# Kernel tuning notes

Measured on AMD Instinct MI355X. Metric: run time of the kernel, lower is better.

## Reference

```python
import jax, jax.numpy as jnp
import numpy as np

H = 12          # num attention heads
D = 768         # hidden size
DH = D // H     # head dim = 64

def setup_inputs() -> dict:
    key = jax.random.key(0)
    ks = jax.random.split(key, 9)
    B, N = 8, 1024
    s = 0.02
    return {
        "hidden_states": jax.random.normal(ks[0], (B, N, D), jnp.float32),
        "Wq": jax.random.normal(ks[1], (D, D), jnp.float32) * s,
        "bq": jnp.zeros((D,), jnp.float32),
        "Wk": jax.random.normal(ks[2], (D, D), jnp.float32) * s,
        "bk": jnp.zeros((D,), jnp.float32),
        "Wv": jax.random.normal(ks[3], (D, D), jnp.float32) * s,
        "bv": jnp.zeros((D,), jnp.float32),
        "Wo": jax.random.normal(ks[4], (D, D), jnp.float32) * s,
        "bo": jnp.zeros((D,), jnp.float32),
    }

def _split_heads(x):
    # [B, N, D] -> [B, H, N, DH]
    B, N, _ = x.shape
    return x.reshape(B, N, H, DH).transpose(0, 2, 1, 3)

def reference(hidden_states, Wq, bq, Wk, bk, Wv, bv, Wo, bo):
    # torch Linear: y = x @ W.T + b
    q = _split_heads(hidden_states @ Wq.T + bq)
    k = _split_heads(hidden_states @ Wk.T + bk)
    v = _split_heads(hidden_states @ Wv.T + bv)
    scale = 1.0 / jnp.sqrt(jnp.asarray(DH, hidden_states.dtype))
    scores = jnp.einsum("bhqd,bhkd->bhqk", q, k) * scale
    probs = jax.nn.softmax(scores, axis=-1)
    ctx = jnp.einsum("bhqk,bhkd->bhqd", probs, v)
    B, _, N, _ = ctx.shape
    ctx = ctx.transpose(0, 2, 1, 3).reshape(B, N, D)
    return ctx @ Wo.T + bo
```

## Files before the change

kernel.cpp:

```cpp
#include <hip/hip_runtime.h>

typedef unsigned short u16;
typedef unsigned int   u32;
typedef unsigned long long u64;
typedef __attribute__((ext_vector_type(8))) short bf16x8;
typedef __attribute__((ext_vector_type(4))) float f32x4;
typedef __attribute__((address_space(3))) u32 lds_u32;
typedef __attribute__((address_space(1))) u32 gbl_u32;

#define MFMA16(a,b,c) __builtin_amdgcn_mfma_f32_16x16x32_bf16((a),(b),(c),0,0,0)
#define QSCALE 0.1803368801111204f

#define WAIT3 do{ asm volatile("s_waitcnt vmcnt(3)" ::: "memory"); }while(0)
#define WAIT4 do{ asm volatile("s_waitcnt vmcnt(4)" ::: "memory"); }while(0)
#define WAIT0 do{ asm volatile("s_waitcnt vmcnt(0)" ::: "memory"); }while(0)
#define SCHED __builtin_amdgcn_sched_barrier(0)
#define BARR  __builtin_amdgcn_s_barrier()

__device__ __forceinline__ u16 f2bf(float f){
  u32 u = __builtin_bit_cast(u32, f);
  u32 r = u + 0x7fffu + ((u>>16)&1u);
  return (u16)(r>>16);
}
__device__ __forceinline__ float bf2f(u16 h){
  return __builtin_bit_cast(float, (u32)h<<16);
}

union V8 { u16 s[8]; uint4 v; };

__global__ __launch_bounds__(256) void cvt_all(const float* __restrict__ hs,
    const float* __restrict__ Wq, const float* __restrict__ Wk,
    const float* __restrict__ Wv, const float* __restrict__ Wo,
    u16* __restrict__ hsb, u16* __restrict__ wqkv, u16* __restrict__ woh)
{
  const int bid = blockIdx.x;
  if (bid < 3072){
    int i = bid*256 + threadIdx.x;
    const float4* p = (const float4*)(hs + (size_t)i*8);
    float4 a = p[0], b = p[1];
    V8 t;
    t.s[0]=f2bf(a.x); t.s[1]=f2bf(a.y); t.s[2]=f2bf(a.z); t.s[3]=f2bf(a.w);
    t.s[4]=f2bf(b.x); t.s[5]=f2bf(b.y); t.s[6]=f2bf(b.z); t.s[7]=f2bf(b.w);
    *(uint4*)(hsb + (size_t)i*8) = t.v;
    return;
  }
  const int r = bid - 3072;
  const int seg = r / 288;
  const int off = (r - seg*288)*256 + threadIdx.x;
  const float* src = seg==0?Wq: seg==1?Wk: seg==2?Wv: Wo;
  const float4* p = (const float4*)(src + (size_t)off*8);
  float4 a = p[0], b = p[1];
  float xs[8] = {a.x,a.y,a.z,a.w,b.x,b.y,b.z,b.w};
  V8 t;
  #pragma unroll
  for (int j=0;j<8;++j) t.s[j]=f2bf(xs[j]);
  if (seg < 3) *(uint4*)(wqkv + (size_t)seg*589824 + (size_t)off*8) = t.v;
  else         *(uint4*)(woh  + (size_t)off*8) = t.v;
}

__global__ __launch_bounds__(512) void mm_qkv(const u16* __restrict__ A, const u16* __restrict__ Bp,
    const float* __restrict__ bq, const float* __restrict__ bk, const float* __restrict__ bvv,
    u16* __restrict__ Oq, u16* __restrict__ Ok, u16* __restrict__ Ov)
{
  __shared__ u16 P[3][12288];
  const int bid = blockIdx.x;
  const int sid = (bid & 7)*72 + (bid >> 3);
  const int mb = sid/9, nb = sid - mb*9;
  const int m0 = mb*128, n0 = nb*256;
  const int tid = threadIdx.x;
  const int lane = tid&63, wid = tid>>6;
  const int wr = wid>>2, wc = wid&3;
  const int fr = lane&15, fg = lane>>4;

  const char* Ab = (const char*)A;
  const char* Bb = (const char*)Bp;
  const char* sp[3];
  #pragma unroll
  for (int c=0;c<3;++c){
    int ci = c*512 + tid;
    if (ci < 512){
      int line = ci>>3, slot = ci&7;
      int d = slot ^ (line&7);
      int row = 2*line + (d>>2);
      sp[c] = Ab + (size_t)(m0+row)*1536 + (d&3)*16;
    } else {
      int i = ci - 512;
      int line = i>>3, slot = i&7;
      int d = slot ^ (line&7);
      int row = 2*line + (d>>2);
      sp[c] = Bb + (size_t)(n0+row)*1536 + (d&3)*16;
    }
  }
  const int sl = (((fr&1)<<2) + fg) ^ (fr>>1);
  const int aoff = (fr&~1)*64 + sl*16 + wr*4096;
  const int boff = 8192 + (fr&~1)*64 + sl*16 + wc*4096;

  f32x4 zz = {0.f,0.f,0.f,0.f};
  f32x4 acc[4][4];
  #pragma unroll
  for (int i=0;i<4;++i)
    #pragma unroll
    for (int j=0;j<4;++j) acc[i][j]=zz;

  auto STAGE = [&](int t, int b){
    char* dst0 = (char*)P[b];
    #pragma unroll
    for (int c=0;c<3;++c)
      __builtin_amdgcn_global_load_lds((const gbl_u32*)(sp[c] + (size_t)t*64),
        (lds_u32*)(dst0 + c*8192 + wid*1024), 16, 0, 0);
  };
  auto COMPUTE = [&](int b){
    const char* pb = (const char*)P[b];
    bf16x8 bfr[4];
    #pragma unroll
    for (int nt=0;nt<4;++nt)
      bfr[nt] = *(const bf16x8*)(pb + boff + nt*1024);
    #pragma unroll
    for (int mt=0;mt<4;++mt){
      bf16x8 af = *(const bf16x8*)(pb + aoff + mt*1024);
      #pragma unroll
      for (int nt=0;nt<4;++nt)
        acc[mt][nt] = MFMA16(af, bfr[nt], acc[mt][nt]);
    }
  };

  STAGE(0, 0); STAGE(1, 1);
  int cb = 0;
  for (int t=0; t<24; ++t){
    if (t < 23) WAIT3; else WAIT0;
    BARR; SCHED;
    if (t < 22){
      int sb = cb + 2; if (sb >= 3) sb -= 3;
      STAGE(t+2, sb);
    }
    __builtin_amdgcn_s_setprio(1);
    COMPUTE(cb);
    __builtin_amdgcn_s_setprio(0);
    cb = (cb == 2) ? 0 : cb + 1;
  }

  const int seg = nb/3;
  const float* bias = seg==0?bq: seg==1?bk:bvv;
  const float sc = (seg==0) ? QSCALE : 1.0f;
  if (seg < 2){
    u16* O = seg==0?Oq:Ok;
    #pragma unroll
    for (int mt=0;mt<4;++mt){
      #pragma unroll
      for (int nt=0;nt<4;++nt){
        int colw = n0 + wc*64 + nt*16 + fr - seg*768;
        float bz = bias[colw];
        int hh = colw>>6, d = colw&63;
        #pragma unroll
        for (int rr=0;rr<4;++rr){
          int row = m0 + wr*64 + mt*16 + fg*4 + rr;
          int b = row>>10, nn = row&1023;
          O[((size_t)(b*12+hh)<<16) + (size_t)nn*64 + d] = f2bf((acc[mt][nt][rr] + bz) * sc);
        }
      }
    }
  } else {
    #pragma unroll
    for (int mt=0;mt<4;++mt){
      #pragma unroll
      for (int nt=0;nt<4;++nt){
        int colw = n0 + wc*64 + nt*16 + fr - 1536;
        float bz = bias[colw];
        int hh = colw>>6, d = colw&63;
        int row0 = m0 + wr*64 + mt*16 + fg*4;
        int b = row0>>10, nn = row0&1023;
        union { u16 h[4]; u64 q; } pk;
        #pragma unroll
        for (int rr=0;rr<4;++rr) pk.h[rr] = f2bf(acc[mt][nt][rr] + bz);
        *(u64*)&Ov[((size_t)(b*12+hh)<<16) + (size_t)d*1024 + nn] = pk.q;
      }
    }
  }
}

__global__ __launch_bounds__(256) void mm_o(const u16* __restrict__ A, const u16* __restrict__ Bp,
                                            const float* __restrict__ bias, float* __restrict__ O)
{
  __shared__ u16 P[3][8192];
  const int bid = blockIdx.x;
  const int sid = (bid & 7)*48 + (bid >> 3);
  const int mb = sid/6, nb = sid - mb*6;
  const int m0 = mb*128, n0 = nb*128;
  const int tid = threadIdx.x;
  const int lane = tid&63, wid = tid>>6;
  const int wr = wid>>1, wc = wid&1;
  const int fr = lane&15, fg = lane>>4;

  const char* Ab = (const char*)A;
  const char* Bb = (const char*)Bp;
  const char* sp[4];
  #pragma unroll
  for (int c=0;c<4;++c){
    int ci = c*256 + tid;
    int row = ci>>3, slot = ci&7;
    int d = slot ^ (row&7);
    if (d < 4) sp[c] = Ab + (size_t)(m0+row)*1536 + d*16;
    else       sp[c] = Bb + (size_t)(n0+row)*1536 + (d-4)*16;
  }
  const int sA = (fg ^ (fr&7)) << 4;
  const int sB = sA ^ 64;

  f32x4 zz = {0.f,0.f,0.f,0.f};
  f32x4 acc[4][4];
  #pragma unroll
  for (int i=0;i<4;++i)
    #pragma unroll
    for (int j=0;j<4;++j) acc[i][j]=zz;

  auto STAGE = [&](int t, int b){
    char* dst0 = (char*)P[b];
    #pragma unroll
    for (int c=0;c<4;++c)
      __builtin_amdgcn_global_load_lds((const gbl_u32*)(sp[c] + (size_t)t*64),
        (lds_u32*)(dst0 + c*4096 + wid*1024), 16, 0, 0);
  };
  auto COMPUTE = [&](int b){
    const char* pb = (const char*)P[b];
    bf16x8 bfr[4];
    #pragma unroll
    for (int nt=0;nt<4;++nt)
      bfr[nt] = *(const bf16x8*)(pb + (wc*64+nt*16+fr)*128 + sB);
    #pragma unroll
    for (int mt=0;mt<4;++mt){
      bf16x8 af = *(const bf16x8*)(pb + (wr*64+mt*16+fr)*128 + sA);
      #pragma unroll
      for (int nt=0;nt<4;++nt)
        acc[mt][nt] = MFMA16(af, bfr[nt], acc[mt][nt]);
    }
  };

  STAGE(0, 0); STAGE(1, 1);
  int cb = 0;
  for (int t=0; t<24; ++t){
    if (t < 23) WAIT4; else WAIT0;
    BARR; SCHED;
    if (t < 22){
      int sb = cb + 2; if (sb >= 3) sb -= 3;
      STAGE(t+2, sb);
    }
    __builtin_amdgcn_s_setprio(1);
    COMPUTE(cb);
    __builtin_amdgcn_s_setprio(0);
    cb = (cb == 2) ? 0 : cb + 1;
  }

  #pragma unroll
  for (int mt=0;mt<4;++mt){
    #pragma unroll
    for (int nt=0;nt<4;++nt){
      int colb = n0 + wc*64 + nt*16 + fr;
      float bz = bias[colb];
      #pragma unroll
      for (int rr=0;rr<4;++rr){
        int row = m0 + wr*64 + mt*16 + fg*4 + rr;
        O[(size_t)row*768 + colb] = acc[mt][nt][rr] + bz;
      }
    }
  }
}

__global__ __launch_bounds__(256) void attn(const u16* __restrict__ qh, const u16* __restrict__ kh,
                                            const u16* __restrict__ vh, u16* __restrict__ ch)
{
  __shared__ u16 Kb[2][4096];
  __shared__ u16 Vb[2][4096];
  __shared__ u16 Ps[4][32][72];
  const int tid=threadIdx.x, w=tid>>6, lane=tid&63;
  const int fr=lane&15, fg=lane>>4;
  const int bh=blockIdx.x, qt=blockIdx.y;
  const size_t base=(size_t)bh<<16;
  const int q0=qt*128 + w*32;

  const char* kbase = (const char*)(kh + base);
  const char* vbase = (const char*)(vh + base);

  int koff[2], voff[2];
  #pragma unroll
  for (int c=0;c<2;++c){
    int ci = c*256 + tid;
    int row = ci>>3;
    int colp = ((ci&7)*16) ^ ((row&7)<<4);
    koff[c] = row*128  + colp;
    voff[c] = row*2048 + colp;
  }

  bf16x8 qf[2][2];
  #pragma unroll
  for (int mt=0;mt<2;++mt)
    #pragma unroll
    for (int ks=0;ks<2;++ks)
      qf[mt][ks] = *(const bf16x8*)&qh[base + (size_t)(q0+mt*16+fr)*64 + ks*32 + fg*8];

  const int swz = (fr&7)<<4;
  int lowD[2];
  #pragma unroll
  for (int ks=0;ks<2;++ks) lowD[ks] = (ks*64 + fg*16) ^ swz;
  const int frbase = fr*128;

  f32x4 zz = {0.f,0.f,0.f,0.f};
  f32x4 o[2][4];
  float lr[2] = {0.f, 0.f};
  #pragma unroll
  for (int mt=0;mt<2;++mt)
    #pragma unroll
    for (int j=0;j<4;++j) o[mt][j]=zz;

  {
    #pragma unroll
    for (int c=0;c<2;++c){
      __builtin_amdgcn_global_load_lds((const gbl_u32*)(kbase + koff[c]),
        (lds_u32*)((char*)&Kb[0][0] + c*4096 + w*1024), 16, 0, 0);
      __builtin_amdgcn_global_load_lds((const gbl_u32*)(vbase + voff[c]),
        (lds_u32*)((char*)&Vb[0][0] + c*4096 + w*1024), 16, 0, 0);
    }
  }
  __syncthreads();

  for (int kt=0; kt<16; ++kt){
    const int buf = kt & 1;
    {
      const int ktn = (kt+1) & 15;
      const char* kt_ = kbase + ktn*8192;
      const char* vt_ = vbase + ktn*128;
      #pragma unroll
      for (int c=0;c<2;++c){
        __builtin_amdgcn_global_load_lds((const gbl_u32*)(kt_ + koff[c]),
          (lds_u32*)((char*)&Kb[buf^1][0] + c*4096 + w*1024), 16, 0, 0);
        __builtin_amdgcn_global_load_lds((const gbl_u32*)(vt_ + voff[c]),
          (lds_u32*)((char*)&Vb[buf^1][0] + c*4096 + w*1024), 16, 0, 0);
      }
    }

    f32x4 s[2][4];
    #pragma unroll
    for (int mt=0;mt<2;++mt)
      #pragma unroll
      for (int j=0;j<4;++j) s[mt][j]=zz;
    const char* kb = (const char*)&Kb[buf][0];
    __builtin_amdgcn_s_setprio(1);
    #pragma unroll
    for (int ct=0;ct<4;++ct){
      #pragma unroll
      for (int ks=0;ks<2;++ks){
        bf16x8 kf = *(const bf16x8*)(kb + ct*2048 + frbase + lowD[ks]);
        s[0][ct]=MFMA16(kf,qf[0][ks],s[0][ct]);
        s[1][ct]=MFMA16(kf,qf[1][ks],s[1][ct]);
      }
    }
    __builtin_amdgcn_s_setprio(0);

    #pragma unroll
    for (int mt=0;mt<2;++mt){
      float lsum = 0.f;
      #pragma unroll
      for (int ct=0;ct<4;++ct){
        float e0 = __builtin_amdgcn_exp2f(s[mt][ct][0]);
        float e1 = __builtin_amdgcn_exp2f(s[mt][ct][1]);
        float e2 = __builtin_amdgcn_exp2f(s[mt][ct][2]);
        float e3 = __builtin_amdgcn_exp2f(s[mt][ct][3]);
        lsum += (e0+e1)+(e2+e3);
        u32 w0, w1;
        asm("v_cvt_pk_bf16_f32 %0, %1, %2" : "=v"(w0) : "v"(e0), "v"(e1));
        asm("v_cvt_pk_bf16_f32 %0, %1, %2" : "=v"(w1) : "v"(e2), "v"(e3));
        uint2 pk2; pk2.x = w0; pk2.y = w1;
        *(uint2*)&Ps[w][mt*16+fr][ct*16+fg*4] = pk2;
      }
      lr[mt] += lsum;
    }

    const char* vb = (const char*)&Vb[buf][0];
    __builtin_amdgcn_s_setprio(1);
    #pragma unroll
    for (int ks2=0;ks2<2;++ks2){
      bf16x8 vf[4];
      #pragma unroll
      for (int dt=0;dt<4;++dt)
        vf[dt] = *(const bf16x8*)(vb + dt*2048 + frbase + lowD[ks2]);
      #pragma unroll
      for (int mt=0;mt<2;++mt){
        bf16x8 pa = *(const bf16x8*)&Ps[w][mt*16+fr][ks2*32+fg*8];
        #pragma unroll
        for (int dt=0;dt<4;++dt)
          o[mt][dt]=MFMA16(pa, vf[dt], o[mt][dt]);
      }
    }
    __builtin_amdgcn_s_setprio(0);

    __syncthreads();
  }

  float inv[2][4];
  #pragma unroll
  for (int mt=0;mt<2;++mt){
    float l = lr[mt];
    l += __shfl_xor(l,16); l += __shfl_xor(l,32);
    #pragma unroll
    for (int rr=0;rr<4;++rr)
      inv[mt][rr] = 1.0f / __shfl(l, fg*4+rr, 16);
  }
  const int b=bh/12, hd=bh%12;
  #pragma unroll
  for (int mt=0;mt<2;++mt){
    #pragma unroll
    for (int dt=0;dt<4;++dt){
      int d = dt*16 + fr;
      #pragma unroll
      for (int rr=0;rr<4;++rr){
        int n = q0 + mt*16 + fg*4 + rr;
        ch[((size_t)b*1024 + n)*768 + hd*64 + d] = f2bf(o[mt][dt][rr] * inv[mt][rr]);
      }
    }
  }
}

extern "C" void kernel_launch(void* const* d_in, const int* in_sizes, int n_in,
                              void* d_out, int out_size, void* d_ws, size_t ws_size,
                              hipStream_t stream) {
  const float* hs = (const float*)d_in[0];
  const float* Wq = (const float*)d_in[1];
  const float* bq = (const float*)d_in[2];
  const float* Wk = (const float*)d_in[3];
  const float* bk = (const float*)d_in[4];
  const float* Wv = (const float*)d_in[5];
  const float* bv = (const float*)d_in[6];
  const float* Wo = (const float*)d_in[7];
  const float* bo = (const float*)d_in[8];
  float* out = (float*)d_out;

  const size_t PS = (size_t)8192*768;
  u16* ws16  = (u16*)d_ws;
  u16* hs_bf = ws16;
  u16* q_bf  = ws16 + PS;
  u16* k_bf  = ws16 + 2*PS;
  u16* v_bf  = ws16 + 3*PS;
  u16* wqkv  = ws16 + 4*PS;
  u16* woh   = wqkv + 3*589824;
  u16* c_hi  = hs_bf;

  dim3 blk(256);
  cvt_all<<<3072 + 4*288, blk, 0, stream>>>(hs, Wq, Wk, Wv, Wo, hs_bf, wqkv, woh);
  mm_qkv<<<576, dim3(512), 0, stream>>>(hs_bf, wqkv, bq, bk, bv, q_bf, k_bf, v_bf);
  attn<<<dim3(96,8), blk, 0, stream>>>(q_bf, k_bf, v_bf, c_hi);
  mm_o<<<384, blk, 0, stream>>>(c_hi, woh, bo, out);
}
```

Before: 115.4 us.

## Deepen QKV GEMM LDS pipeline to four stages with ping-pong phase structure

The QKV projection GEMM goes from a triple-buffered LDS pipeline to a quad-buffered one that prefetches three K-tiles ahead. The main loop is unrolled into two phases per iteration. Each phase loads all A/B fragments from LDS into registers, issues the next global-to-LDS stage, then waits and barriers before a dense MFMA block. The aim is to overlap global loads with compute and keep LDS reads apart from MFMA issue. In exchange it uses more LDS, which may lower occupancy, and adds extra barriers.

```diff
diff --git a/kernel.cpp b/kernel.cpp
--- a/kernel.cpp
+++ b/kernel.cpp
@@ -14,6 +14,7 @@
 #define WAIT3 do{ asm volatile("s_waitcnt vmcnt(3)" ::: "memory"); }while(0)
 #define WAIT4 do{ asm volatile("s_waitcnt vmcnt(4)" ::: "memory"); }while(0)
 #define WAIT0 do{ asm volatile("s_waitcnt vmcnt(0)" ::: "memory"); }while(0)
+#define LGK0  do{ asm volatile("s_waitcnt lgkmcnt(0)" ::: "memory"); }while(0)
 #define SCHED __builtin_amdgcn_sched_barrier(0)
 #define BARR  __builtin_amdgcn_s_barrier()
 
@@ -62,7 +63,7 @@
     const float* __restrict__ bq, const float* __restrict__ bk, const float* __restrict__ bvv,
     u16* __restrict__ Oq, u16* __restrict__ Ok, u16* __restrict__ Ov)
 {
-  __shared__ u16 P[3][12288];
+  __shared__ u16 P[4][12288];
   const int bid = blockIdx.x;
   const int sid = (bid & 7)*72 + (bid >> 3);
   const int mb = sid/9, nb = sid - mb*9;
@@ -102,41 +103,41 @@
     #pragma unroll
     for (int j=0;j<4;++j) acc[i][j]=zz;
 
-  auto STAGE = [&](int t, int b){
-    char* dst0 = (char*)P[b];
+  auto STAGE = [&](int s, int idx){
+    char* dst0 = (char*)P[idx];
     #pragma unroll
     for (int c=0;c<3;++c)
-      __builtin_amdgcn_global_load_lds((const gbl_u32*)(sp[c] + (size_t)t*64),
+      __builtin_amdgcn_global_load_lds((const gbl_u32*)(sp[c] + (size_t)s*64),
         (lds_u32*)(dst0 + c*8192 + wid*1024), 16, 0, 0);
   };
-  auto COMPUTE = [&](int b){
-    const char* pb = (const char*)P[b];
-    bf16x8 bfr[4];
-    #pragma unroll
-    for (int nt=0;nt<4;++nt)
-      bfr[nt] = *(const bf16x8*)(pb + boff + nt*1024);
-    #pragma unroll
-    for (int mt=0;mt<4;++mt){
-      bf16x8 af = *(const bf16x8*)(pb + aoff + mt*1024);
+  auto PHASE = [&](const char* hb, int s, int idx, int wait){
+    bf16x8 bfr[4], af[4];
+    #pragma unroll
+    for (int nt=0;nt<4;++nt) bfr[nt] = *(const bf16x8*)(hb + boff + nt*1024);
+    #pragma unroll
+    for (int mt=0;mt<4;++mt) af[mt] = *(const bf16x8*)(hb + aoff + mt*1024);
+    if (s >= 0) STAGE(s, idx);
+    if (wait == 3) WAIT3; else if (wait == 0) WAIT0;
+    SCHED; BARR;
+    LGK0; SCHED;
+    __builtin_amdgcn_s_setprio(1);
+    #pragma unroll
+    for (int mt=0;mt<4;++mt)
       #pragma unroll
       for (int nt=0;nt<4;++nt)
-        acc[mt][nt] = MFMA16(af, bfr[nt], acc[mt][nt]);
-    }
+        acc[mt][nt] = MFMA16(af[mt], bfr[nt], acc[mt][nt]);
+    __builtin_amdgcn_s_setprio(0);
+    SCHED; BARR;
   };
 
-  STAGE(0, 0); STAGE(1, 1);
-  int cb = 0;
-  for (int t=0; t<24; ++t){
-    if (t < 23) WAIT3; else WAIT0;
-    BARR; SCHED;
-    if (t < 22){
-      int sb = cb + 2; if (sb >= 3) sb -= 3;
-      STAGE(t+2, sb);
-    }
-    __builtin_amdgcn_s_setprio(1);
-    COMPUTE(cb);
-    __builtin_amdgcn_s_setprio(0);
-    cb = (cb == 2) ? 0 : cb + 1;
+  STAGE(0, 0); STAGE(1, 1); STAGE(2, 2);
+  WAIT3; SCHED; BARR;
+
+  for (int t=0; t<12; ++t){
+    const char* h0 = (const char*)P[(2*t)&3];
+    const char* h1 = (const char*)P[(2*t+1)&3];
+    PHASE(h0, (t<11)? (2*t+3) : -1, (2*t+3)&3, -1);
+    PHASE(h1, (t<10)? (2*t+4) : -1, (2*t+4)&3, (t<10)? 3 : (t==10 ? 0 : -1));
   }
 
   const int seg = nb/3;
```

Result: slower. 123.4 us (+6.9%).

## Load V fragments directly from global into registers, drop V LDS staging

Applied to the files above, without the earlier changes.

The attention kernel no longer stages the transposed V tile through double-buffered shared memory. Each wave now reads its V fragments straight from global memory into registers at the start of each key tile, and the launch bounds request 4 blocks per CU. This removes the LDS traffic and footprint for V so more blocks can be resident. In exchange, the four waves of a block each re-read the same V data from global or cache, and those loads are issued in the same iteration they are consumed, so their latency may not be fully hidden.

```diff
diff --git a/kernel.cpp b/kernel.cpp
--- a/kernel.cpp
+++ b/kernel.cpp
@@ -264,11 +264,10 @@
   }
 }
 
-__global__ __launch_bounds__(256) void attn(const u16* __restrict__ qh, const u16* __restrict__ kh,
-                                            const u16* __restrict__ vh, u16* __restrict__ ch)
+__global__ __launch_bounds__(256, 4) void attn(const u16* __restrict__ qh, const u16* __restrict__ kh,
+                                               const u16* __restrict__ vh, u16* __restrict__ ch)
 {
   __shared__ u16 Kb[2][4096];
-  __shared__ u16 Vb[2][4096];
   __shared__ u16 Ps[4][32][72];
   const int tid=threadIdx.x, w=tid>>6, lane=tid&63;
   const int fr=lane&15, fg=lane>>4;
@@ -277,16 +276,15 @@
   const int q0=qt*128 + w*32;
 
   const char* kbase = (const char*)(kh + base);
-  const char* vbase = (const char*)(vh + base);
-
-  int koff[2], voff[2];
+  const u16*  vg    = vh + base;
+
+  int koff[2];
   #pragma unroll
   for (int c=0;c<2;++c){
     int ci = c*256 + tid;
     int row = ci>>3;
     int colp = ((ci&7)*16) ^ ((row&7)<<4);
-    koff[c] = row*128  + colp;
-    voff[c] = row*2048 + colp;
+    koff[c] = row*128 + colp;
   }
 
   bf16x8 qf[2][2];
@@ -312,12 +310,9 @@
 
   {
     #pragma unroll
-    for (int c=0;c<2;++c){
+    for (int c=0;c<2;++c)
       __builtin_amdgcn_global_load_lds((const gbl_u32*)(kbase + koff[c]),
         (lds_u32*)((char*)&Kb[0][0] + c*4096 + w*1024), 16, 0, 0);
-      __builtin_amdgcn_global_load_lds((const gbl_u32*)(vbase + voff[c]),
-        (lds_u32*)((char*)&Vb[0][0] + c*4096 + w*1024), 16, 0, 0);
-    }
   }
   __syncthreads();
 
@@ -326,15 +321,16 @@
     {
       const int ktn = (kt+1) & 15;
       const char* kt_ = kbase + ktn*8192;
-      const char* vt_ = vbase + ktn*128;
-      #pragma unroll
-      for (int c=0;c<2;++c){
+      #pragma unroll
+      for (int c=0;c<2;++c)
         __builtin_amdgcn_global_load_lds((const gbl_u32*)(kt_ + koff[c]),
           (lds_u32*)((char*)&Kb[buf^1][0] + c*4096 + w*1024), 16, 0, 0);
-        __builtin_amdgcn_global_load_lds((const gbl_u32*)(vt_ + voff[c]),
-          (lds_u32*)((char*)&Vb[buf^1][0] + c*4096 + w*1024), 16, 0, 0);
-      }
-    }
+    }
+
+    bf16x8 vf0[4];
+    #pragma unroll
+    for (int dt=0;dt<4;++dt)
+      vf0[dt] = *(const bf16x8*)&vg[(size_t)(dt*16+fr)*1024 + kt*64 + fg*8];
 
     f32x4 s[2][4];
     #pragma unroll
@@ -373,21 +369,25 @@
       lr[mt] += lsum;
     }
 
-    const char* vb = (const char*)&Vb[buf][0];
+    bf16x8 vf1[4];
+    #pragma unroll
+    for (int dt=0;dt<4;++dt)
+      vf1[dt] = *(const bf16x8*)&vg[(size_t)(dt*16+fr)*1024 + kt*64 + 32 + fg*8];
+
     __builtin_amdgcn_s_setprio(1);
     #pragma unroll
-    for (int ks2=0;ks2<2;++ks2){
-      bf16x8 vf[4];
+    for (int mt=0;mt<2;++mt){
+      bf16x8 pa = *(const bf16x8*)&Ps[w][mt*16+fr][fg*8];
       #pragma unroll
       for (int dt=0;dt<4;++dt)
-        vf[dt] = *(const bf16x8*)(vb + dt*2048 + frbase + lowD[ks2]);
-      #pragma unroll
-      for (int mt=0;mt<2;++mt){
-        bf16x8 pa = *(const bf16x8*)&Ps[w][mt*16+fr][ks2*32+fg*8];
-        #pragma unroll
-        for (int dt=0;dt<4;++dt)
-          o[mt][dt]=MFMA16(pa, vf[dt], o[mt][dt]);
-      }
+        o[mt][dt]=MFMA16(pa, vf0[dt], o[mt][dt]);
+    }
+    #pragma unroll
+    for (int mt=0;mt<2;++mt){
+      bf16x8 pa = *(const bf16x8*)&Ps[w][mt*16+fr][32+fg*8];
+      #pragma unroll
+      for (int dt=0;dt<4;++dt)
+        o[mt][dt]=MFMA16(pa, vf1[dt], o[mt][dt]);
     }
     __builtin_amdgcn_s_setprio(0);
 
```

Result: slower. 140.8 us (+21.9%).
